# Performance work log

Hardware: AMD Instinct MI355X
Metric: run time of the kernel (lower is better)

The kernel has to match this reference:

```python
import jax, jax.numpy as jnp
import numpy as np

NUM_UNITS = 32   # nodes per graph (obs_dim 160 / 5)
B = 2048         # graphs per batch
FEAT_IN = 5
NUM_OUT = 5


def setup_inputs() -> dict:
    key = jax.random.key(0)
    ks = jax.random.split(key, 16)
    obs = jax.random.normal(ks[0], (B, NUM_UNITS * FEAT_IN), dtype=jnp.float32)
    # Fully-connected (incl. self-loop) edge list per graph, offset by graph id.
    i = jnp.arange(NUM_UNITS, dtype=jnp.int32)
    s, d = jnp.meshgrid(i, i, indexing='ij')          # all 32x32 pairs
    offs = (jnp.arange(B, dtype=jnp.int32) * NUM_UNITS)[:, None]
    src = (s.reshape(-1)[None, :] + offs).reshape(-1)  # [B*1024]
    dst = (d.reshape(-1)[None, :] + offs).reshape(-1)
    def lin(k, fin, fout):
        return jax.random.normal(k, (fout, fin), dtype=jnp.float32) * (1.0 / np.sqrt(fin))
    return {
        'obs': obs, 'src': src, 'dst': dst,
        'W1l': lin(ks[1], 5, 64),  'b1': jnp.zeros((64,), jnp.float32),  'W1r': lin(ks[2], 5, 64),
        'W2l': lin(ks[3], 64, 128), 'b2': jnp.zeros((128,), jnp.float32), 'W2r': lin(ks[4], 64, 128),
        'W3l': lin(ks[5], 128, 128), 'b3': jnp.zeros((128,), jnp.float32), 'W3r': lin(ks[6], 128, 128),
        'Wp': lin(ks[7], 128, NUM_OUT), 'bp': jnp.zeros((NUM_OUT,), jnp.float32),
    }


def reference(obs, src, dst, W1l, b1, W1r, W2l, b2, W2r, W3l, b3, W3r, Wp, bp):
    x = obs.reshape(-1, FEAT_IN)                 # [N, 5], N = B*32
    N = x.shape[0]
    deg = jnp.float32(NUM_UNITS)                 # every node has 32 in-edges

    def sage(h, Wl, b, Wr):
        # PyG SAGEConv: lin_l(mean_{j->i} h_j) + lin_r(h_i); bias lives in lin_l
        msg = h[src]                             # gather  [E, F]
        agg = jax.ops.segment_sum(msg, dst, num_segments=N) / deg
        return agg @ Wl.T + b + h @ Wr.T

    h = jax.nn.relu(sage(x, W1l, b1, W1r))
    h = jax.nn.relu(sage(h, W2l, b2, W2r))
    h = jax.nn.relu(sage(h, W3l, b3, W3r))
    pooled = h.reshape(B, NUM_UNITS, 128).mean(axis=1)   # global_mean_pool (equal-size graphs)
    return pooled @ Wp.T + bp                    # policy_out [B, NUM_OUT]
```

## Files before the change

kernel.cpp:

```cpp
#include <hip/hip_runtime.h>
#include <hip/hip_bf16.h>


typedef float f32x4 __attribute__((ext_vector_type(4)));
typedef __bf16 bf16x8 __attribute__((ext_vector_type(8)));

__device__ __forceinline__ f32x4 MFMA(bf16x8 a, bf16x8 b, f32x4 c) {
  return __builtin_amdgcn_mfma_f32_16x16x32_bf16(a, b, c, 0, 0, 0);
}

__device__ __forceinline__ unsigned short bfbits(float v) {
  __hip_bfloat16 t = __float2bfloat16(v);
  return __builtin_bit_cast(unsigned short, t);
}

__device__ __forceinline__ bf16x8 pack8(f32x4 lo, f32x4 hi) {
  union { bf16x8 v; unsigned short u[8]; } t;
  t.u[0] = bfbits(lo[0]); t.u[1] = bfbits(lo[1]);
  t.u[2] = bfbits(lo[2]); t.u[3] = bfbits(lo[3]);
  t.u[4] = bfbits(hi[0]); t.u[5] = bfbits(hi[1]);
  t.u[6] = bfbits(hi[2]); t.u[7] = bfbits(hi[3]);
  return t.v;
}

__global__ __launch_bounds__(256) void gnn_prep(
    const float* __restrict__ W1l, const float* __restrict__ W1r,
    const float* __restrict__ W2l, const float* __restrict__ W2r,
    const float* __restrict__ W3l, const float* __restrict__ W3r,
    unsigned short* __restrict__ wpack)
{
  int e = blockIdx.x * 256 + threadIdx.x;
  if (e >= 53248) return;
  const float* src; int Kreal, KS, eloc;
  if      (e < 2048)  { src = W1r; Kreal = 5;   KS = 1; eloc = e; }
  else if (e < 4096)  { src = W1l; Kreal = 5;   KS = 1; eloc = e - 2048; }
  else if (e < 12288) { src = W2r; Kreal = 64;  KS = 2; eloc = e - 4096; }
  else if (e < 20480) { src = W2l; Kreal = 64;  KS = 2; eloc = e - 12288; }
  else if (e < 36864) { src = W3r; Kreal = 128; KS = 4; eloc = e - 20480; }
  else                { src = W3l; Kreal = 128; KS = 4; eloc = e - 36864; }
  int j = eloc & 7, lane = (eloc >> 3) & 63, rest = eloc >> 9;
  int ks = rest % KS, ft = rest / KS;
  int f = ft * 16 + (lane & 15);
  int k = ks * 32 + (lane >> 4) * 8 + j;
  float v = (k < Kreal) ? src[f * Kreal + k] : 0.f;
  wpack[e] = bfbits(v);
}

#define RBS 36

__device__ __forceinline__ void qpass(float* rb, float* mb, int lane, int fbase,
                                      f32x4 t00, f32x4 t01, f32x4 t10, f32x4 t11,
                                      bf16x8* Bn0, bf16x8* Bn1, bf16x8* Bg) {
  const int g = lane >> 4, c = lane & 15;
  *(f32x4*)(rb + c * RBS + 4 * g)              = t00;
  *(f32x4*)(rb + c * RBS + 16 + 4 * g)         = t01;
  *(f32x4*)(rb + (16 + c) * RBS + 4 * g)       = t10;
  *(f32x4*)(rb + (16 + c) * RBS + 16 + 4 * g)  = t11;
  const int qd = lane & 7, rg = lane >> 3;
  f32x4 s = {0.f, 0.f, 0.f, 0.f};
#pragma unroll
  for (int rr = 0; rr < 4; ++rr)
    s += *(const f32x4*)(rb + (rg * 4 + rr) * RBS + qd * 4);
#pragma unroll
  for (int i = 0; i < 4; ++i) {
    float v = s[i];
    v += __shfl_xor(v, 8, 64); v += __shfl_xor(v, 16, 64); v += __shfl_xor(v, 32, 64);
    s[i] = v * 0.03125f;
  }
  if (lane < 8) *(f32x4*)(mb + fbase + qd * 4) = s;
  if (Bn0) {
    f32x4 lo0 = *(const f32x4*)(rb + c * RBS + 8 * g);
    f32x4 hi0 = *(const f32x4*)(rb + c * RBS + 8 * g + 4);
    *Bn0 = pack8(lo0, hi0);
    f32x4 lo1 = *(const f32x4*)(rb + (16 + c) * RBS + 8 * g);
    f32x4 hi1 = *(const f32x4*)(rb + (16 + c) * RBS + 8 * g + 4);
    *Bn1 = pack8(lo1, hi1);
    f32x4 glo = *(const f32x4*)(mb + fbase + 8 * g);
    f32x4 ghi = *(const f32x4*)(mb + fbase + 8 * g + 4);
    *Bg = pack8(glo, ghi);
  }
}

__global__ __launch_bounds__(512) void gnn_fused(
    const float* __restrict__ obs,
    const float* __restrict__ b1, const float* __restrict__ b2,
    const float* __restrict__ b3,
    const float* __restrict__ Wp, const float* __restrict__ bp,
    const unsigned short* __restrict__ wpack,
    float* __restrict__ out)
{
  __shared__ unsigned short smW[32768];
  __shared__ float rb_all[8][32 * RBS];
  __shared__ float mb_all[8][128];

  const int tid  = threadIdx.x;
  const int wid  = tid >> 6;
  const int lane = tid & 63;
  const int g    = lane >> 4;
  const int c    = lane & 15;
  float* rb = &rb_all[wid][0];
  float* mb = &mb_all[wid][0];
  const int graph = blockIdx.x * 8 + wid;
  const float* xg = obs + graph * 160;

  const unsigned short* A1r = wpack;
  const unsigned short* A1l = wpack + 2048;
  const unsigned short* A2r = wpack + 4096;
  const unsigned short* A2l = wpack + 12288;

  bf16x8 ar1[4], al1[4];
#pragma unroll
  for (int ft = 0; ft < 4; ++ft) {
    ar1[ft] = *(const bf16x8*)(A1r + (ft * 64 + lane) * 8);
    al1[ft] = *(const bf16x8*)(A1l + (ft * 64 + lane) * 8);
  }
  float x0[5], x1[5];
#pragma unroll
  for (int j = 0; j < 5; ++j) { x0[j] = xg[c * 5 + j]; x1[j] = xg[80 + c * 5 + j]; }

  {
    const unsigned short* gA3 = wpack + 20480;
#pragma unroll
    for (int it = 0; it < 8; ++it) {
      const int chunk = it * 8 + wid;
      const void* gsrc = (const void*)((const char*)(gA3 + chunk * 512) + lane * 16);
      __builtin_amdgcn_global_load_lds(
          (const __attribute__((address_space(1))) unsigned int*)gsrc,
          (__attribute__((address_space(3))) unsigned int*)&smW[chunk * 512],
          16, 0, 0);
    }
  }

  const f32x4 Z4 = {0.f, 0.f, 0.f, 0.f};

  float m0[5];
#pragma unroll
  for (int j = 0; j < 5; ++j) {
    float s = x0[j] + x1[j];
    s += __shfl_xor(s, 1, 64); s += __shfl_xor(s, 2, 64);
    s += __shfl_xor(s, 4, 64); s += __shfl_xor(s, 8, 64);
    m0[j] = s * 0.03125f;
  }
  bf16x8 Bn1[2], Bg1;
  {
    f32x4 a0 = {x0[0], x0[1], x0[2], x0[3]}, a1 = {x0[4], 0.f, 0.f, 0.f};
    f32x4 n0 = {x1[0], x1[1], x1[2], x1[3]}, n1 = {x1[4], 0.f, 0.f, 0.f};
    f32x4 g0 = {m0[0], m0[1], m0[2], m0[3]}, g1 = {m0[4], 0.f, 0.f, 0.f};
    if (g != 0) { a0 = Z4; a1 = Z4; n0 = Z4; n1 = Z4; g0 = Z4; g1 = Z4; }
    Bn1[0] = pack8(a0, a1); Bn1[1] = pack8(n0, n1); Bg1 = pack8(g0, g1);
  }

  f32x4 acc[2][8];
#pragma unroll
  for (int ft = 0; ft < 4; ++ft) {
    f32x4 bias = *(const f32x4*)(b1 + ft * 16 + 4 * g);
    acc[0][ft] = bias; acc[1][ft] = bias;
    acc[0][ft] = MFMA(ar1[ft], Bn1[0], acc[0][ft]);
    acc[1][ft] = MFMA(ar1[ft], Bn1[1], acc[1][ft]);
    acc[0][ft] = MFMA(al1[ft], Bg1, acc[0][ft]);
    acc[1][ft] = MFMA(al1[ft], Bg1, acc[1][ft]);
  }
#pragma unroll
  for (int ct = 0; ct < 2; ++ct)
#pragma unroll
    for (int ft = 0; ft < 4; ++ft)
#pragma unroll
      for (int i = 0; i < 4; ++i)
        acc[ct][ft][i] = fmaxf(acc[ct][ft][i], 0.f);

  bf16x8 Bn2[2][2], Bg2[2];
  qpass(rb, mb, lane, 0,  acc[0][0], acc[0][1], acc[1][0], acc[1][1],
        &Bn2[0][0], &Bn2[1][0], &Bg2[0]);
  qpass(rb, mb, lane, 32, acc[0][2], acc[0][3], acc[1][2], acc[1][3],
        &Bn2[0][1], &Bn2[1][1], &Bg2[1]);

#pragma unroll
  for (int ft = 0; ft < 8; ++ft) {
    f32x4 bias = *(const f32x4*)(b2 + ft * 16 + 4 * g);
    acc[0][ft] = bias; acc[1][ft] = bias;
#pragma unroll
    for (int ks = 0; ks < 2; ++ks) {
      bf16x8 ar = *(const bf16x8*)(A2r + ((ft * 2 + ks) * 64 + lane) * 8);
      bf16x8 al = *(const bf16x8*)(A2l + ((ft * 2 + ks) * 64 + lane) * 8);
      acc[0][ft] = MFMA(ar, Bn2[0][ks], acc[0][ft]);
      acc[1][ft] = MFMA(ar, Bn2[1][ks], acc[1][ft]);
      acc[0][ft] = MFMA(al, Bg2[ks], acc[0][ft]);
      acc[1][ft] = MFMA(al, Bg2[ks], acc[1][ft]);
    }
  }
#pragma unroll
  for (int ct = 0; ct < 2; ++ct)
#pragma unroll
    for (int ft = 0; ft < 8; ++ft)
#pragma unroll
      for (int i = 0; i < 4; ++i)
        acc[ct][ft][i] = fmaxf(acc[ct][ft][i], 0.f);

  bf16x8 Bn3[2][4], Bg3[4];
#pragma unroll
  for (int ks = 0; ks < 4; ++ks)
    qpass(rb, mb, lane, 32 * ks,
          acc[0][2 * ks], acc[0][2 * ks + 1], acc[1][2 * ks], acc[1][2 * ks + 1],
          &Bn3[0][ks], &Bn3[1][ks], &Bg3[ks]);

  asm volatile("s_waitcnt vmcnt(0)" ::: "memory");
  __syncthreads();

  {
    const unsigned short* A3r = smW;
    const unsigned short* A3l = smW + 16384;
#pragma unroll
    for (int ft = 0; ft < 8; ++ft) {
      f32x4 bias = *(const f32x4*)(b3 + ft * 16 + 4 * g);
      acc[0][ft] = bias; acc[1][ft] = bias;
#pragma unroll
      for (int ks = 0; ks < 4; ++ks) {
        bf16x8 ar = *(const bf16x8*)(A3r + ((ft * 4 + ks) * 64 + lane) * 8);
        bf16x8 al = *(const bf16x8*)(A3l + ((ft * 4 + ks) * 64 + lane) * 8);
        acc[0][ft] = MFMA(ar, Bn3[0][ks], acc[0][ft]);
        acc[1][ft] = MFMA(ar, Bn3[1][ks], acc[1][ft]);
        acc[0][ft] = MFMA(al, Bg3[ks], acc[0][ft]);
        acc[1][ft] = MFMA(al, Bg3[ks], acc[1][ft]);
      }
    }
  }
#pragma unroll
  for (int ct = 0; ct < 2; ++ct)
#pragma unroll
    for (int ft = 0; ft < 8; ++ft)
#pragma unroll
      for (int i = 0; i < 4; ++i)
        acc[ct][ft][i] = fmaxf(acc[ct][ft][i], 0.f);

#pragma unroll
  for (int ks = 0; ks < 4; ++ks)
    qpass(rb, mb, lane, 32 * ks,
          acc[0][2 * ks], acc[0][2 * ks + 1], acc[1][2 * ks], acc[1][2 * ks + 1],
          nullptr, nullptr, nullptr);

  float p0 = mb[lane], p1 = mb[64 + lane];
  float po[5];
#pragma unroll
  for (int o = 0; o < 5; ++o)
    po[o] = p0 * Wp[o * 128 + lane] + p1 * Wp[o * 128 + 64 + lane];
#pragma unroll
  for (int o = 0; o < 5; ++o) {
    float v = po[o];
    v += __shfl_xor(v, 1, 64);  v += __shfl_xor(v, 2, 64);
    v += __shfl_xor(v, 4, 64);  v += __shfl_xor(v, 8, 64);
    v += __shfl_xor(v, 16, 64); v += __shfl_xor(v, 32, 64);
    po[o] = v;
  }
  if (lane == 0) {
#pragma unroll
    for (int o = 0; o < 5; ++o) out[graph * 5 + o] = po[o] + bp[o];
  }
}

extern "C" void kernel_launch(void* const* d_in, const int* in_sizes, int n_in,
                              void* d_out, int out_size, void* d_ws, size_t ws_size,
                              hipStream_t stream)
{
  const float* obs = (const float*)d_in[0];
  const float* W1l = (const float*)d_in[3];
  const float* b1  = (const float*)d_in[4];
  const float* W1r = (const float*)d_in[5];
  const float* W2l = (const float*)d_in[6];
  const float* b2  = (const float*)d_in[7];
  const float* W2r = (const float*)d_in[8];
  const float* W3l = (const float*)d_in[9];
  const float* b3  = (const float*)d_in[10];
  const float* W3r = (const float*)d_in[11];
  const float* Wp  = (const float*)d_in[12];
  const float* bp  = (const float*)d_in[13];
  unsigned short* wpack = (unsigned short*)d_ws;
  float* out = (float*)d_out;

  gnn_prep<<<208, 256, 0, stream>>>(W1l, W1r, W2l, W2r, W3l, W3r, wpack);
  gnn_fused<<<256, 512, 0, stream>>>(obs, b1, b2, b3, Wp, bp, wpack, out);
}
```

Baseline: 24.22 us.

## Stage layer activations in LDS as bf16 and compute means with shuffles

Replaces the fp32 LDS round-trip (qpass) with a bf16 staging buffer holding the full activation tile, converting to bf16 before the store so the B fragments can be loaded directly as bf16x8. Column means are now computed with cross-lane shuffle reductions on registers instead of re-reading the LDS tile. Layer-1 weight loads are moved next to their MFMAs to reduce register pressure. This trades LDS traffic and conversion work for more shuffle instructions (16 shuffles per fragment instead of 3).

```diff
diff --git a/kernel.cpp b/kernel.cpp
--- a/kernel.cpp
+++ b/kernel.cpp
@@ -4,6 +4,7 @@
 
 typedef float f32x4 __attribute__((ext_vector_type(4)));
 typedef __bf16 bf16x8 __attribute__((ext_vector_type(8)));
+typedef unsigned short u16x4 __attribute__((ext_vector_type(4)));
 
 __device__ __forceinline__ f32x4 MFMA(bf16x8 a, bf16x8 b, f32x4 c) {
   return __builtin_amdgcn_mfma_f32_16x16x32_bf16(a, b, c, 0, 0, 0);
@@ -12,6 +13,13 @@
 __device__ __forceinline__ unsigned short bfbits(float v) {
   __hip_bfloat16 t = __float2bfloat16(v);
   return __builtin_bit_cast(unsigned short, t);
+}
+
+__device__ __forceinline__ u16x4 pack4(f32x4 v) {
+  u16x4 r;
+  r[0] = bfbits(v[0]); r[1] = bfbits(v[1]);
+  r[2] = bfbits(v[2]); r[3] = bfbits(v[3]);
+  return r;
 }
 
 __device__ __forceinline__ bf16x8 pack8(f32x4 lo, f32x4 hi) {
@@ -46,40 +54,7 @@
   wpack[e] = bfbits(v);
 }
 
-#define RBS 36
-
-__device__ __forceinline__ void qpass(float* rb, float* mb, int lane, int fbase,
-                                      f32x4 t00, f32x4 t01, f32x4 t10, f32x4 t11,
-                                      bf16x8* Bn0, bf16x8* Bn1, bf16x8* Bg) {
-  const int g = lane >> 4, c = lane & 15;
-  *(f32x4*)(rb + c * RBS + 4 * g)              = t00;
-  *(f32x4*)(rb + c * RBS + 16 + 4 * g)         = t01;
-  *(f32x4*)(rb + (16 + c) * RBS + 4 * g)       = t10;
-  *(f32x4*)(rb + (16 + c) * RBS + 16 + 4 * g)  = t11;
-  const int qd = lane & 7, rg = lane >> 3;
-  f32x4 s = {0.f, 0.f, 0.f, 0.f};
-#pragma unroll
-  for (int rr = 0; rr < 4; ++rr)
-    s += *(const f32x4*)(rb + (rg * 4 + rr) * RBS + qd * 4);
-#pragma unroll
-  for (int i = 0; i < 4; ++i) {
-    float v = s[i];
-    v += __shfl_xor(v, 8, 64); v += __shfl_xor(v, 16, 64); v += __shfl_xor(v, 32, 64);
-    s[i] = v * 0.03125f;
-  }
-  if (lane < 8) *(f32x4*)(mb + fbase + qd * 4) = s;
-  if (Bn0) {
-    f32x4 lo0 = *(const f32x4*)(rb + c * RBS + 8 * g);
-    f32x4 hi0 = *(const f32x4*)(rb + c * RBS + 8 * g + 4);
-    *Bn0 = pack8(lo0, hi0);
-    f32x4 lo1 = *(const f32x4*)(rb + (16 + c) * RBS + 8 * g);
-    f32x4 hi1 = *(const f32x4*)(rb + (16 + c) * RBS + 8 * g + 4);
-    *Bn1 = pack8(lo1, hi1);
-    f32x4 glo = *(const f32x4*)(mb + fbase + 8 * g);
-    f32x4 ghi = *(const f32x4*)(mb + fbase + 8 * g + 4);
-    *Bg = pack8(glo, ghi);
-  }
-}
+#define RBW 136
 
 __global__ __launch_bounds__(512) void gnn_fused(
     const float* __restrict__ obs,
@@ -90,16 +65,18 @@
     float* __restrict__ out)
 {
   __shared__ unsigned short smW[32768];
-  __shared__ float rb_all[8][32 * RBS];
-  __shared__ float mb_all[8][128];
+  __shared__ unsigned short rb_all[8][32 * RBW];
+  __shared__ unsigned short mb_all[8][128];
+  __shared__ float mbf_all[8][128];
 
   const int tid  = threadIdx.x;
   const int wid  = tid >> 6;
   const int lane = tid & 63;
   const int g    = lane >> 4;
   const int c    = lane & 15;
-  float* rb = &rb_all[wid][0];
-  float* mb = &mb_all[wid][0];
+  unsigned short* rbb = &rb_all[wid][0];
+  unsigned short* mbb = &mb_all[wid][0];
+  float* mbf = &mbf_all[wid][0];
   const int graph = blockIdx.x * 8 + wid;
   const float* xg = obs + graph * 160;
 
@@ -107,16 +84,6 @@
   const unsigned short* A1l = wpack + 2048;
   const unsigned short* A2r = wpack + 4096;
   const unsigned short* A2l = wpack + 12288;
-
-  bf16x8 ar1[4], al1[4];
-#pragma unroll
-  for (int ft = 0; ft < 4; ++ft) {
-    ar1[ft] = *(const bf16x8*)(A1r + (ft * 64 + lane) * 8);
-    al1[ft] = *(const bf16x8*)(A1l + (ft * 64 + lane) * 8);
-  }
-  float x0[5], x1[5];
-#pragma unroll
-  for (int j = 0; j < 5; ++j) { x0[j] = xg[c * 5 + j]; x1[j] = xg[80 + c * 5 + j]; }
 
   {
     const unsigned short* gA3 = wpack + 20480;
@@ -133,6 +100,9 @@
 
   const f32x4 Z4 = {0.f, 0.f, 0.f, 0.f};
 
+  float x0[5], x1[5];
+#pragma unroll
+  for (int j = 0; j < 5; ++j) { x0[j] = xg[c * 5 + j]; x1[j] = xg[80 + c * 5 + j]; }
   float m0[5];
 #pragma unroll
   for (int j = 0; j < 5; ++j) {
@@ -155,10 +125,12 @@
   for (int ft = 0; ft < 4; ++ft) {
     f32x4 bias = *(const f32x4*)(b1 + ft * 16 + 4 * g);
     acc[0][ft] = bias; acc[1][ft] = bias;
-    acc[0][ft] = MFMA(ar1[ft], Bn1[0], acc[0][ft]);
-    acc[1][ft] = MFMA(ar1[ft], Bn1[1], acc[1][ft]);
-    acc[0][ft] = MFMA(al1[ft], Bg1, acc[0][ft]);
-    acc[1][ft] = MFMA(al1[ft], Bg1, acc[1][ft]);
+    bf16x8 ar = *(const bf16x8*)(A1r + (ft * 64 + lane) * 8);
+    bf16x8 al = *(const bf16x8*)(A1l + (ft * 64 + lane) * 8);
+    acc[0][ft] = MFMA(ar, Bn1[0], acc[0][ft]);
+    acc[1][ft] = MFMA(ar, Bn1[1], acc[1][ft]);
+    acc[0][ft] = MFMA(al, Bg1, acc[0][ft]);
+    acc[1][ft] = MFMA(al, Bg1, acc[1][ft]);
   }
 #pragma unroll
   for (int ct = 0; ct < 2; ++ct)
@@ -168,11 +140,30 @@
       for (int i = 0; i < 4; ++i)
         acc[ct][ft][i] = fmaxf(acc[ct][ft][i], 0.f);
 
-  bf16x8 Bn2[2][2], Bg2[2];
-  qpass(rb, mb, lane, 0,  acc[0][0], acc[0][1], acc[1][0], acc[1][1],
-        &Bn2[0][0], &Bn2[1][0], &Bg2[0]);
-  qpass(rb, mb, lane, 32, acc[0][2], acc[0][3], acc[1][2], acc[1][3],
-        &Bn2[0][1], &Bn2[1][1], &Bg2[1]);
+#pragma unroll
+  for (int ft = 0; ft < 4; ++ft) {
+    *(u16x4*)(rbb + c * RBW        + ft * 16 + 4 * g) = pack4(acc[0][ft]);
+    *(u16x4*)(rbb + (16 + c) * RBW + ft * 16 + 4 * g) = pack4(acc[1][ft]);
+    f32x4 s = acc[0][ft] + acc[1][ft];
+#pragma unroll
+    for (int i = 0; i < 4; ++i) {
+      float v = s[i];
+      v += __shfl_xor(v, 1, 64); v += __shfl_xor(v, 2, 64);
+      v += __shfl_xor(v, 4, 64); v += __shfl_xor(v, 8, 64);
+      s[i] = v * 0.03125f;
+    }
+    if (c == 0) *(u16x4*)(mbb + ft * 16 + 4 * g) = pack4(s);
+  }
+
+  bf16x8 Bn[2][4], Bg[4];
+#pragma unroll
+  for (int ct = 0; ct < 2; ++ct)
+#pragma unroll
+    for (int ks = 0; ks < 2; ++ks)
+      Bn[ct][ks] = *(const bf16x8*)(rbb + (ct * 16 + c) * RBW + 32 * ks + 8 * g);
+#pragma unroll
+  for (int ks = 0; ks < 2; ++ks)
+    Bg[ks] = *(const bf16x8*)(mbb + 32 * ks + 8 * g);
 
 #pragma unroll
   for (int ft = 0; ft < 8; ++ft) {
@@ -182,10 +173,10 @@
     for (int ks = 0; ks < 2; ++ks) {
       bf16x8 ar = *(const bf16x8*)(A2r + ((ft * 2 + ks) * 64 + lane) * 8);
       bf16x8 al = *(const bf16x8*)(A2l + ((ft * 2 + ks) * 64 + lane) * 8);
-      acc[0][ft] = MFMA(ar, Bn2[0][ks], acc[0][ft]);
-      acc[1][ft] = MFMA(ar, Bn2[1][ks], acc[1][ft]);
-      acc[0][ft] = MFMA(al, Bg2[ks], acc[0][ft]);
-      acc[1][ft] = MFMA(al, Bg2[ks], acc[1][ft]);
+      acc[0][ft] = MFMA(ar, Bn[0][ks], acc[0][ft]);
+      acc[1][ft] = MFMA(ar, Bn[1][ks], acc[1][ft]);
+      acc[0][ft] = MFMA(al, Bg[ks], acc[0][ft]);
+      acc[1][ft] = MFMA(al, Bg[ks], acc[1][ft]);
     }
   }
 #pragma unroll
@@ -196,12 +187,29 @@
       for (int i = 0; i < 4; ++i)
         acc[ct][ft][i] = fmaxf(acc[ct][ft][i], 0.f);
 
-  bf16x8 Bn3[2][4], Bg3[4];
+#pragma unroll
+  for (int ft = 0; ft < 8; ++ft) {
+    *(u16x4*)(rbb + c * RBW        + ft * 16 + 4 * g) = pack4(acc[0][ft]);
+    *(u16x4*)(rbb + (16 + c) * RBW + ft * 16 + 4 * g) = pack4(acc[1][ft]);
+    f32x4 s = acc[0][ft] + acc[1][ft];
+#pragma unroll
+    for (int i = 0; i < 4; ++i) {
+      float v = s[i];
+      v += __shfl_xor(v, 1, 64); v += __shfl_xor(v, 2, 64);
+      v += __shfl_xor(v, 4, 64); v += __shfl_xor(v, 8, 64);
+      s[i] = v * 0.03125f;
+    }
+    if (c == 0) *(u16x4*)(mbb + ft * 16 + 4 * g) = pack4(s);
+  }
+
+#pragma unroll
+  for (int ct = 0; ct < 2; ++ct)
+#pragma unroll
+    for (int ks = 0; ks < 4; ++ks)
+      Bn[ct][ks] = *(const bf16x8*)(rbb + (ct * 16 + c) * RBW + 32 * ks + 8 * g);
 #pragma unroll
   for (int ks = 0; ks < 4; ++ks)
-    qpass(rb, mb, lane, 32 * ks,
-          acc[0][2 * ks], acc[0][2 * ks + 1], acc[1][2 * ks], acc[1][2 * ks + 1],
-          &Bn3[0][ks], &Bn3[1][ks], &Bg3[ks]);
+    Bg[ks] = *(const bf16x8*)(mbb + 32 * ks + 8 * g);
 
   asm volatile("s_waitcnt vmcnt(0)" ::: "memory");
   __syncthreads();
@@ -217,10 +225,10 @@
       for (int ks = 0; ks < 4; ++ks) {
         bf16x8 ar = *(const bf16x8*)(A3r + ((ft * 4 + ks) * 64 + lane) * 8);
         bf16x8 al = *(const bf16x8*)(A3l + ((ft * 4 + ks) * 64 + lane) * 8);
-        acc[0][ft] = MFMA(ar, Bn3[0][ks], acc[0][ft]);
-        acc[1][ft] = MFMA(ar, Bn3[1][ks], acc[1][ft]);
-        acc[0][ft] = MFMA(al, Bg3[ks], acc[0][ft]);
-        acc[1][ft] = MFMA(al, Bg3[ks], acc[1][ft]);
+        acc[0][ft] = MFMA(ar, Bn[0][ks], acc[0][ft]);
+        acc[1][ft] = MFMA(ar, Bn[1][ks], acc[1][ft]);
+        acc[0][ft] = MFMA(al, Bg[ks], acc[0][ft]);
+        acc[1][ft] = MFMA(al, Bg[ks], acc[1][ft]);
       }
     }
   }
@@ -233,12 +241,19 @@
         acc[ct][ft][i] = fmaxf(acc[ct][ft][i], 0.f);
 
 #pragma unroll
-  for (int ks = 0; ks < 4; ++ks)
-    qpass(rb, mb, lane, 32 * ks,
-          acc[0][2 * ks], acc[0][2 * ks + 1], acc[1][2 * ks], acc[1][2 * ks + 1],
-          nullptr, nullptr, nullptr);
-
-  float p0 = mb[lane], p1 = mb[64 + lane];
+  for (int ft = 0; ft < 8; ++ft) {
+    f32x4 s = acc[0][ft] + acc[1][ft];
+#pragma unroll
+    for (int i = 0; i < 4; ++i) {
+      float v = s[i];
+      v += __shfl_xor(v, 1, 64); v += __shfl_xor(v, 2, 64);
+      v += __shfl_xor(v, 4, 64); v += __shfl_xor(v, 8, 64);
+      s[i] = v * 0.03125f;
+    }
+    if (c == 0) *(f32x4*)(mbf + ft * 16 + 4 * g) = s;
+  }
+
+  float p0 = mbf[lane], p1 = mbf[64 + lane];
   float po[5];
 #pragma unroll
   for (int o = 0; o < 5; ++o)
```

Measured after the change: 26.86 us. 10.9% more time.
